# Kernel optimization log

Hardware: AMD Instinct MI355X
Metric: run time of the kernel (lower is better)

Reference implementation:

```python
import jax, jax.numpy as jnp
import numpy as np

N_NODES = 50000
N_EDGES = 1_600_000
FEAT, HIDDEN, NUM_CLASS = 128, 128, 64


def setup_inputs() -> dict:
    key = jax.random.key(0)
    k1, k2, k3, k4, k5 = jax.random.split(key, 5)
    h = jax.random.normal(k1, (N_NODES, FEAT), dtype=jnp.float32)
    edge_index = jax.random.randint(k2, (2, N_EDGES), 0, N_NODES, dtype=jnp.int32)
    # Glorot-ish init for the three GraphConv weights (bias=False)
    W1 = jax.random.normal(k3, (FEAT, HIDDEN), dtype=jnp.float32) * (1.0 / np.sqrt(FEAT))
    W2 = jax.random.normal(k4, (HIDDEN, HIDDEN), dtype=jnp.float32) * (1.0 / np.sqrt(HIDDEN))
    W3 = jax.random.normal(k5, (HIDDEN, NUM_CLASS), dtype=jnp.float32) * (1.0 / np.sqrt(HIDDEN))
    return {"h": h, "edge_index": edge_index, "W1": W1, "W2": W2, "W3": W3}


def _gcn_layer(h, W, src, dst, out_isqrt, in_isqrt, n_nodes):
    # DGL GraphConv, norm='both', bias=False: relu( D_in^{-1/2} A D_out^{-1/2} h W )
    h = h * out_isqrt[:, None]          # scale source features
    h = h @ W                            # dense projection (order-invariant)
    agg = jax.ops.segment_sum(h[src], dst, num_segments=n_nodes)  # SpMM aggregation
    agg = agg * in_isqrt[:, None]
    return jax.nn.relu(agg)


def reference(h, edge_index, W1, W2, W3):
    src, dst = edge_index[0], edge_index[1]
    ones = jnp.ones(src.shape[0], dtype=h.dtype)
    out_deg = jax.ops.segment_sum(ones, src, num_segments=N_NODES)
    in_deg = jax.ops.segment_sum(ones, dst, num_segments=N_NODES)
    out_isqrt = jnp.clip(out_deg, 1.0, None) ** -0.5
    in_isqrt = jnp.clip(in_deg, 1.0, None) ** -0.5
    h = _gcn_layer(h, W1, src, dst, out_isqrt, in_isqrt, N_NODES)
    h = _gcn_layer(h, W2, src, dst, out_isqrt, in_isqrt, N_NODES)
    h = _gcn_layer(h, W3, src, dst, out_isqrt, in_isqrt, N_NODES)
    return h
```

## Files before the change

kernel.cpp:

```cpp
#include <hip/hip_runtime.h>

#define N_NODES 50000
#define N_EDGES 1600000
#define FEAT 128
#define HIDDEN 128
#define NUM_CLASS 64

#define NBUCK 782
#define EPB 2048
#define NBLK 782
#define SCAP 2560
#define AGG_NBN 3125
#define GEMM_BLOCKS 782
#define NSHW 6256

typedef _Float16 h8 __attribute__((ext_vector_type(8)));
typedef _Float16 h4 __attribute__((ext_vector_type(4)));
typedef float f32x4 __attribute__((ext_vector_type(4)));

__global__ __launch_bounds__(256) void passA_kernel(const int* __restrict__ ei,
                                                    unsigned* __restrict__ priv,
                                                    int* __restrict__ localoff,
                                                    int* __restrict__ Cmat,
                                                    unsigned* __restrict__ nibshad) {
    __shared__ int cnt[1024];
    __shared__ int base[1024];
    __shared__ int cur[1024];
    __shared__ int tmp[256];
    __shared__ unsigned sorted[EPB];
    __shared__ unsigned nib[NSHW];
    const int t = threadIdx.x;
    const int blk = blockIdx.x;
    for (int i = t; i < 1024; i += 256) cnt[i] = 0;
    for (int i = t; i < NSHW; i += 256) nib[i] = 0;
    __syncthreads();

    const int ebase = blk * EPB;
    unsigned packed[8];
    int bk[8];
#pragma unroll
    for (int j = 0; j < 8; ++j) {
        const int e = ebase + t + j * 256;
        if (e < N_EDGES) {
            const unsigned s = (unsigned)ei[e];
            const unsigned d = (unsigned)ei[N_EDGES + e];
            bk[j] = (int)(d >> 6);
            packed[j] = s | ((d & 63u) << 16) | ((d >> 6) << 22);
            atomicAdd(&cnt[bk[j]], 1);
            atomicAdd(&nib[s >> 3], 1u << ((s & 7u) * 4u));
        } else bk[j] = -1;
    }
    __syncthreads();

    const int c0 = cnt[4*t], c1 = cnt[4*t+1], c2 = cnt[4*t+2], c3 = cnt[4*t+3];
    const int s = c0 + c1 + c2 + c3;
    tmp[t] = s;
    __syncthreads();
    for (int off = 1; off < 256; off <<= 1) {
        int v = (t >= off) ? tmp[t - off] : 0;
        __syncthreads();
        tmp[t] += v;
        __syncthreads();
    }
    const int excl = tmp[t] - s;
    base[4*t] = excl;            cur[4*t] = excl;
    base[4*t+1] = excl+c0;       cur[4*t+1] = excl+c0;
    base[4*t+2] = excl+c0+c1;    cur[4*t+2] = excl+c0+c1;
    base[4*t+3] = excl+c0+c1+c2; cur[4*t+3] = excl+c0+c1+c2;
    __syncthreads();

    for (int b = t; b < NBUCK; b += 256) {
        localoff[(size_t)blk * NBUCK + b] = base[b];
        Cmat[(size_t)blk * NBUCK + b] = cnt[b];
    }
#pragma unroll
    for (int j = 0; j < 8; ++j)
        if (bk[j] >= 0) {
            const int pos = atomicAdd(&cur[bk[j]], 1);
            sorted[pos] = packed[j];
        }
    __syncthreads();
    const int total = min(EPB, N_EDGES - ebase);
    for (int i = t; i < total; i += 256) priv[(size_t)blk * EPB + i] = sorted[i];
    unsigned* dst = nibshad + (size_t)blk * NSHW;
    for (int i = t; i < NSHW; i += 256) dst[i] = nib[i];
}

__global__ __launch_bounds__(256) void btotal_kernel(const int* __restrict__ Cmat,
                                                     int* __restrict__ total) {
    const int b0 = blockIdx.x * 4;
    const int t = threadIdx.x;
    const int c = t & 3, r = t >> 2;
    int s = 0;
    if (b0 + c < NBUCK)
        for (int i = r; i < NBLK; i += 64) s += Cmat[(size_t)i * NBUCK + b0 + c];
    __shared__ int red[256];
    red[t] = s;
    __syncthreads();
    for (int off = 128; off >= 4; off >>= 1) {
        if (t < off) red[t] += red[t + off];
        __syncthreads();
    }
    if (t < 4 && b0 + t < NBUCK) total[b0 + t] = red[t];
}

__global__ __launch_bounds__(256) void bscan2_kernel(const int* __restrict__ total,
                                                     int* __restrict__ csr_base,
                                                     int* __restrict__ row_off) {
    __shared__ int tt[1024];
    __shared__ int tmp[256];
    const int t = threadIdx.x;
    for (int i = t; i < 1024; i += 256) tt[i] = (i < NBUCK) ? total[i] : 0;
    __syncthreads();
    const int c0 = tt[4*t], c1 = tt[4*t+1], c2 = tt[4*t+2], c3 = tt[4*t+3];
    const int s = c0 + c1 + c2 + c3;
    tmp[t] = s;
    __syncthreads();
    for (int off = 1; off < 256; off <<= 1) {
        int v = (t >= off) ? tmp[t - off] : 0;
        __syncthreads();
        tmp[t] += v;
        __syncthreads();
    }
    const int excl = tmp[t] - s;
    if (4*t < NBUCK)   csr_base[4*t]   = excl;
    if (4*t+1 < NBUCK) csr_base[4*t+1] = excl + c0;
    if (4*t+2 < NBUCK) csr_base[4*t+2] = excl + c0 + c1;
    if (4*t+3 < NBUCK) csr_base[4*t+3] = excl + c0 + c1 + c2;
    if (t == 0) { csr_base[NBUCK] = N_EDGES; row_off[N_NODES] = N_EDGES; }
}

__global__ __launch_bounds__(256) void setup_kernel(const float* __restrict__ W1,
                                                    const float* __restrict__ W2,
                                                    const float* __restrict__ W3,
                                                    _Float16* __restrict__ WhT,
                                                    const unsigned* __restrict__ nibshad,
                                                    float* __restrict__ out_isqrt) {
    const int bid = blockIdx.x;
    const int t = threadIdx.x;
    if (bid < 160) {
        const int id = bid * 256 + t;
        if (id < 16384) {
            const int n = id >> 7, k = id & 127;
            WhT[id] = (_Float16)W1[k * 128 + n];
        } else if (id < 32768) {
            const int i = id - 16384, n = i >> 7, k = i & 127;
            WhT[id] = (_Float16)W2[k * 128 + n];
        } else if (id < 40960) {
            const int i = id - 32768, n = i >> 7, k = i & 127;
            WhT[id] = (_Float16)W3[k * 64 + n];
        }
        return;
    }
    const int blk = bid - 160;
    const int w0 = blk * 8;
    const int wl = t & 7, c = t >> 3;
    int acc[8] = {0, 0, 0, 0, 0, 0, 0, 0};
    for (int sh = c; sh < NBLK; sh += 32) {
        const unsigned u = nibshad[(size_t)sh * NSHW + w0 + wl];
        acc[0] += u & 15u;         acc[1] += (u >> 4) & 15u;
        acc[2] += (u >> 8) & 15u;  acc[3] += (u >> 12) & 15u;
        acc[4] += (u >> 16) & 15u; acc[5] += (u >> 20) & 15u;
        acc[6] += (u >> 24) & 15u; acc[7] += (u >> 28);
    }
    __shared__ int red[32][8][8];
#pragma unroll
    for (int nb = 0; nb < 8; ++nb) red[c][wl][nb] = acc[nb];
    __syncthreads();
    for (int off = 16; off > 0; off >>= 1) {
        if (c < off) {
#pragma unroll
            for (int nb = 0; nb < 8; ++nb) red[c][wl][nb] += red[c + off][wl][nb];
        }
        __syncthreads();
    }
    if (t < 64) {
        const int wl2 = t >> 3, nb = t & 7;
        const int node = (w0 + wl2) * 8 + nb;
        if (node < N_NODES) {
            const int d = red[0][wl2][nb];
            out_isqrt[node] = rsqrtf((float)(d < 1 ? 1 : d));
        }
    }
}

__global__ __launch_bounds__(256) void csr2_kernel(const int* __restrict__ localoff,
                                                   const unsigned* __restrict__ priv,
                                                   const int* __restrict__ csr_base,
                                                   unsigned short* __restrict__ csr,
                                                   int* __restrict__ row_off,
                                                   float* __restrict__ in_isqrt) {
    __shared__ unsigned gath[SCAP];
    __shared__ int tmp[256];
    __shared__ int cnt64[64];
    __shared__ int cur64[64];
    const int b = blockIdx.x;
    const int t = threadIdx.x;

    int off_[4], len_[4];
#pragma unroll
    for (int u = 0; u < 4; ++u) {
        const int blk = 4*t + u;
        if (blk < NBLK) {
            const int o = localoff[(size_t)blk * NBUCK + b];
            const int nxt = (b == NBUCK - 1) ? min(EPB, N_EDGES - blk * EPB)
                                             : localoff[(size_t)blk * NBUCK + b + 1];
            off_[u] = o; len_[u] = nxt - o;
        } else { off_[u] = 0; len_[u] = 0; }
    }
    const int s = len_[0] + len_[1] + len_[2] + len_[3];
    tmp[t] = s;
    __syncthreads();
    for (int off = 1; off < 256; off <<= 1) {
        int v = (t >= off) ? tmp[t - off] : 0;
        __syncthreads();
        tmp[t] += v;
        __syncthreads();
    }
    int run = tmp[t] - s;
    const int total = tmp[255];
#pragma unroll
    for (int u = 0; u < 4; ++u) {
        const int blk = 4*t + u;
        const unsigned* srcp = priv + (size_t)blk * EPB + off_[u];
        for (int j = 0; j < len_[u]; ++j)
            if (run + j < SCAP) gath[run + j] = srcp[j];
        run += len_[u];
    }
    if (t < 64) cnt64[t] = 0;
    __syncthreads();

    const int gtot = min(total, SCAP);
    for (int i = t; i < gtot; i += 256) atomicAdd(&cnt64[(gath[i] >> 16) & 63u], 1);
    __syncthreads();

    const int v64 = (t < 64) ? cnt64[t] : 0;
    tmp[t] = v64;
    __syncthreads();
    for (int off = 1; off < 64; off <<= 1) {
        int v = (t >= off) ? tmp[t - off] : 0;
        __syncthreads();
        tmp[t] += v;
        __syncthreads();
    }
    if (t < 64) {
        const int myoff = csr_base[b] + tmp[t] - v64;
        cur64[t] = myoff;
        const int node = b * 64 + t;
        if (node < N_NODES) {
            row_off[node] = myoff;
            in_isqrt[node] = rsqrtf((float)(v64 > 0 ? v64 : 1));
        }
    }
    __syncthreads();

    for (int i = t; i < gtot; i += 256) {
        const unsigned w = gath[i];
        const int pos = atomicAdd(&cur64[(w >> 16) & 63u], 1);
        csr[pos] = (unsigned short)(w & 0xFFFFu);
    }
}

template <int OUT, typename InT>
__global__ __launch_bounds__(256) void gemm_kernel(const InT* __restrict__ H,
                                                   const _Float16* __restrict__ WhT,
                                                   const float* __restrict__ out_isqrt,
                                                   _Float16* __restrict__ Ys) {
    constexpr int NT = OUT / 16;
    __shared__ _Float16 Hs[64 * 128];
    char* hb = (char*)Hs;
    const int tid = threadIdx.x;
    const int bn = blockIdx.x * 64;

    {
        const int n = tid & 63, kg = tid >> 6;
        const int gn = bn + n;
        const int swz = (n & 7) << 4;
        if (gn < N_NODES) {
            if constexpr (sizeof(InT) == 4) {
                const float4* hrow = (const float4*)(H + (size_t)gn * FEAT) + kg * 8;
#pragma unroll
                for (int jj = 0; jj < 4; ++jj) {
                    const float4 u = hrow[jj * 2];
                    const float4 v = hrow[jj * 2 + 1];
                    h8 r;
                    r[0] = (_Float16)u.x; r[1] = (_Float16)u.y; r[2] = (_Float16)u.z; r[3] = (_Float16)u.w;
                    r[4] = (_Float16)v.x; r[5] = (_Float16)v.y; r[6] = (_Float16)v.z; r[7] = (_Float16)v.w;
                    *(h8*)(hb + ((n * 256 + kg * 64 + jj * 16) ^ swz)) = r;
                }
            } else {
                const h8* hrow = (const h8*)(H + (size_t)gn * FEAT) + kg * 4;
#pragma unroll
                for (int jj = 0; jj < 4; ++jj)
                    *(h8*)(hb + ((n * 256 + kg * 64 + jj * 16) ^ swz)) = hrow[jj];
            }
        } else {
            h8 z;
#pragma unroll
            for (int i = 0; i < 8; ++i) z[i] = (_Float16)0.f;
#pragma unroll
            for (int jj = 0; jj < 4; ++jj)
                *(h8*)(hb + ((n * 256 + kg * 64 + jj * 16) ^ swz)) = z;
        }
    }
    __syncthreads();

    const int l = tid & 63, w = tid >> 6;
    const int lm = l & 15, lk = l >> 4;
    const int nloc = w * 16 + lm;
    const int swzr = (nloc & 7) << 4;

    h8 bfrag[4];
#pragma unroll
    for (int kt = 0; kt < 4; ++kt)
        bfrag[kt] = *(const h8*)(hb + ((nloc * 256 + (lk * 8 + kt * 32) * 2) ^ swzr));

    f32x4 acc[NT];
#pragma unroll
    for (int nt = 0; nt < NT; ++nt) acc[nt] = (f32x4){0.f, 0.f, 0.f, 0.f};

#pragma unroll
    for (int nt = 0; nt < NT; ++nt) {
        const _Float16* wp = WhT + (size_t)(nt * 16 + lm) * 128 + lk * 8;
#pragma unroll
        for (int kt = 0; kt < 4; ++kt) {
            const h8 afrag = *(const h8*)(wp + kt * 32);
            acc[nt] = __builtin_amdgcn_mfma_f32_16x16x32_f16(afrag, bfrag[kt], acc[nt], 0, 0, 0);
        }
    }

    const int node = bn + w * 16 + lm;
    if (node < N_NODES) {
        const float sc = out_isqrt[node];
#pragma unroll
        for (int nt = 0; nt < NT; ++nt) {
            const int f0 = nt * 16 + lk * 4;
            h4 r;
            r[0] = (_Float16)(acc[nt][0] * sc);
            r[1] = (_Float16)(acc[nt][1] * sc);
            r[2] = (_Float16)(acc[nt][2] * sc);
            r[3] = (_Float16)(acc[nt][3] * sc);
            *(h4*)(Ys + ((size_t)(f0 >> 5) * N_NODES + node) * 32 + (f0 & 31)) = r;
        }
    }
}

template <int F, typename OT>
__global__ __launch_bounds__(256) void agg_kernel(const int* __restrict__ row_off,
                                                  const unsigned short* __restrict__ csr,
                                                  const _Float16* __restrict__ Ys,
                                                  const float* __restrict__ in_isqrt,
                                                  OT* __restrict__ out) {
    constexpr int NS = F / 32;
    const int s  = blockIdx.x & (NS - 1);
    const int nb = blockIdx.x / NS;
    const int tid = threadIdx.x;
    const int lane = tid & 63;
    const int j = lane >> 4;
    const int esub = (lane >> 2) & 3;
    const int q = lane & 3;

    const int d = nb * 16 + (tid >> 6) * 4 + j;
    const _Float16* Yp = Ys + (size_t)s * (N_NODES * 32) + q * 8;

    const int end = row_off[d + 1];
    float a0 = 0.f, a1 = 0.f, a2 = 0.f, a3 = 0.f, a4 = 0.f, a5 = 0.f, a6 = 0.f, a7 = 0.f;

    int e = row_off[d] + esub;
    for (; e + 12 < end; e += 16) {
        const int i0 = csr[e];
        const int i1 = csr[e + 4];
        const int i2 = csr[e + 8];
        const int i3 = csr[e + 12];
        const h8 v0 = *(const h8*)(Yp + (size_t)i0 * 32);
        const h8 v1 = *(const h8*)(Yp + (size_t)i1 * 32);
        const h8 v2 = *(const h8*)(Yp + (size_t)i2 * 32);
        const h8 v3 = *(const h8*)(Yp + (size_t)i3 * 32);
        a0 += (float)v0[0] + (float)v1[0] + (float)v2[0] + (float)v3[0];
        a1 += (float)v0[1] + (float)v1[1] + (float)v2[1] + (float)v3[1];
        a2 += (float)v0[2] + (float)v1[2] + (float)v2[2] + (float)v3[2];
        a3 += (float)v0[3] + (float)v1[3] + (float)v2[3] + (float)v3[3];
        a4 += (float)v0[4] + (float)v1[4] + (float)v2[4] + (float)v3[4];
        a5 += (float)v0[5] + (float)v1[5] + (float)v2[5] + (float)v3[5];
        a6 += (float)v0[6] + (float)v1[6] + (float)v2[6] + (float)v3[6];
        a7 += (float)v0[7] + (float)v1[7] + (float)v2[7] + (float)v3[7];
    }
    for (; e + 4 < end; e += 8) {
        const int i0 = csr[e];
        const int i1 = csr[e + 4];
        const h8 v0 = *(const h8*)(Yp + (size_t)i0 * 32);
        const h8 v1 = *(const h8*)(Yp + (size_t)i1 * 32);
        a0 += (float)v0[0] + (float)v1[0];
        a1 += (float)v0[1] + (float)v1[1];
        a2 += (float)v0[2] + (float)v1[2];
        a3 += (float)v0[3] + (float)v1[3];
        a4 += (float)v0[4] + (float)v1[4];
        a5 += (float)v0[5] + (float)v1[5];
        a6 += (float)v0[6] + (float)v1[6];
        a7 += (float)v0[7] + (float)v1[7];
    }
    if (e < end) {
        const int i0 = csr[e];
        const h8 v0 = *(const h8*)(Yp + (size_t)i0 * 32);
        a0 += (float)v0[0]; a1 += (float)v0[1]; a2 += (float)v0[2]; a3 += (float)v0[3];
        a4 += (float)v0[4]; a5 += (float)v0[5]; a6 += (float)v0[6]; a7 += (float)v0[7];
    }

    a0 += __shfl_xor(a0, 4, 64); a0 += __shfl_xor(a0, 8, 64);
    a1 += __shfl_xor(a1, 4, 64); a1 += __shfl_xor(a1, 8, 64);
    a2 += __shfl_xor(a2, 4, 64); a2 += __shfl_xor(a2, 8, 64);
    a3 += __shfl_xor(a3, 4, 64); a3 += __shfl_xor(a3, 8, 64);
    a4 += __shfl_xor(a4, 4, 64); a4 += __shfl_xor(a4, 8, 64);
    a5 += __shfl_xor(a5, 4, 64); a5 += __shfl_xor(a5, 8, 64);
    a6 += __shfl_xor(a6, 4, 64); a6 += __shfl_xor(a6, 8, 64);
    a7 += __shfl_xor(a7, 4, 64); a7 += __shfl_xor(a7, 8, 64);

    if (esub == 0) {
        const float isq = in_isqrt[d];
        const float r0 = fmaxf(a0 * isq, 0.f), r1 = fmaxf(a1 * isq, 0.f);
        const float r2 = fmaxf(a2 * isq, 0.f), r3 = fmaxf(a3 * isq, 0.f);
        const float r4 = fmaxf(a4 * isq, 0.f), r5 = fmaxf(a5 * isq, 0.f);
        const float r6 = fmaxf(a6 * isq, 0.f), r7 = fmaxf(a7 * isq, 0.f);
        if constexpr (sizeof(OT) == 2) {
            h8 o;
            o[0] = (_Float16)r0; o[1] = (_Float16)r1; o[2] = (_Float16)r2; o[3] = (_Float16)r3;
            o[4] = (_Float16)r4; o[5] = (_Float16)r5; o[6] = (_Float16)r6; o[7] = (_Float16)r7;
            *(h8*)((_Float16*)out + (size_t)d * F + s * 32 + q * 8) = o;
        } else {
            float* op = (float*)out + (size_t)d * F + s * 32 + q * 8;
            float4 w0 = {r0, r1, r2, r3}, w1 = {r4, r5, r6, r7};
            *(float4*)op = w0;
            *(float4*)(op + 4) = w1;
        }
    }
}

extern "C" void kernel_launch(void* const* d_in, const int* in_sizes, int n_in,
                              void* d_out, int out_size, void* d_ws, size_t ws_size,
                              hipStream_t stream) {
    const float* h  = (const float*)d_in[0];
    const int*   ei = (const int*)d_in[1];
    const float* W1 = (const float*)d_in[2];
    const float* W2 = (const float*)d_in[3];
    const float* W3 = (const float*)d_in[4];
    float* out = (float*)d_out;

    char* p = (char*)d_ws;
    auto alloc = [&p](size_t bytes) {
        void* r = (void*)p;
        p += (bytes + 255) & ~(size_t)255;
        return r;
    };
    int*   row_off  = (int*)alloc((N_NODES + 1) * sizeof(int));
    int*   csr_base = (int*)alloc((NBUCK + 1) * sizeof(int));
    int*   total    = (int*)alloc(NBUCK * sizeof(int));
    unsigned short* csr = (unsigned short*)alloc((size_t)N_EDGES * sizeof(unsigned short));
    float* in_isqrt  = (float*)alloc(N_NODES * sizeof(float));
    float* out_isqrt = (float*)alloc(N_NODES * sizeof(float));
    _Float16* WhT   = (_Float16*)alloc(40960 * sizeof(_Float16));
    _Float16* Ys    = (_Float16*)alloc((size_t)N_NODES * HIDDEN * sizeof(_Float16));
    _Float16* bufA  = (_Float16*)alloc((size_t)N_NODES * HIDDEN * sizeof(_Float16));
    _Float16* bufB  = (_Float16*)alloc((size_t)N_NODES * HIDDEN * sizeof(_Float16));
    unsigned* nibshad = (unsigned*)alloc((size_t)NBLK * NSHW * sizeof(unsigned));
    unsigned* priv   = (unsigned*)bufA;
    int* localoff    = (int*)bufB;
    int* Cmat        = localoff + (size_t)NBLK * NBUCK;

    passA_kernel<<<NBLK, 256, 0, stream>>>(ei, priv, localoff, Cmat, nibshad);
    btotal_kernel<<<(NBUCK + 3) / 4, 256, 0, stream>>>(Cmat, total);
    bscan2_kernel<<<1, 256, 0, stream>>>(total, csr_base, row_off);
    setup_kernel<<<160 + NBLK, 256, 0, stream>>>(W1, W2, W3, WhT, nibshad, out_isqrt);
    csr2_kernel<<<NBUCK, 256, 0, stream>>>(localoff, priv, csr_base, csr, row_off, in_isqrt);

    gemm_kernel<HIDDEN, float><<<GEMM_BLOCKS, 256, 0, stream>>>(h, WhT, out_isqrt, Ys);
    agg_kernel<HIDDEN, _Float16><<<4 * AGG_NBN, 256, 0, stream>>>(row_off, csr, Ys, in_isqrt, bufA);

    gemm_kernel<HIDDEN, _Float16><<<GEMM_BLOCKS, 256, 0, stream>>>(bufA, WhT + 16384, out_isqrt, Ys);
    agg_kernel<HIDDEN, _Float16><<<4 * AGG_NBN, 256, 0, stream>>>(row_off, csr, Ys, in_isqrt, bufB);

    gemm_kernel<NUM_CLASS, _Float16><<<GEMM_BLOCKS, 256, 0, stream>>>(bufB, WhT + 32768, out_isqrt, Ys);
    agg_kernel<NUM_CLASS, float><<<2 * AGG_NBN, 256, 0, stream>>>(row_off, csr, Ys, in_isqrt, out);
}
```

Baseline: 235.2 us.

## Widen feature slabs to 64 halfs and fold bucket totals into setup kernel

The intermediate Ys layout changes from 32-wide to 64-wide feature slabs. Each aggregation gather now reads a 128-byte contiguous row segment, and each dst node is handled by 32 lanes (8 feature quads × 4 edge subsets) instead of 16. The 16-edge unrolled loop is dropped, and the grid shrinks to match. Separately, the btotal kernel is merged into setup_kernel as extra blocks so there is one fewer launch, with bscan2 run after it. The aims are better gather coalescing and less launch overhead, at the cost of less memory-level parallelism per thread.

Result: slower. 241.6 us (+2.8%).

```diff
diff --git a/kernel.cpp b/kernel.cpp
--- a/kernel.cpp
+++ b/kernel.cpp
@@ -10,7 +10,7 @@
 #define EPB 2048
 #define NBLK 782
 #define SCAP 2560
-#define AGG_NBN 3125
+#define AGG_NBN 6250
 #define GEMM_BLOCKS 782
 #define NSHW 6256
 
@@ -86,51 +86,9 @@
     for (int i = t; i < NSHW; i += 256) dst[i] = nib[i];
 }
 
-__global__ __launch_bounds__(256) void btotal_kernel(const int* __restrict__ Cmat,
-                                                     int* __restrict__ total) {
-    const int b0 = blockIdx.x * 4;
-    const int t = threadIdx.x;
-    const int c = t & 3, r = t >> 2;
-    int s = 0;
-    if (b0 + c < NBUCK)
-        for (int i = r; i < NBLK; i += 64) s += Cmat[(size_t)i * NBUCK + b0 + c];
-    __shared__ int red[256];
-    red[t] = s;
-    __syncthreads();
-    for (int off = 128; off >= 4; off >>= 1) {
-        if (t < off) red[t] += red[t + off];
-        __syncthreads();
-    }
-    if (t < 4 && b0 + t < NBUCK) total[b0 + t] = red[t];
-}
-
-__global__ __launch_bounds__(256) void bscan2_kernel(const int* __restrict__ total,
-                                                     int* __restrict__ csr_base,
-                                                     int* __restrict__ row_off) {
-    __shared__ int tt[1024];
-    __shared__ int tmp[256];
-    const int t = threadIdx.x;
-    for (int i = t; i < 1024; i += 256) tt[i] = (i < NBUCK) ? total[i] : 0;
-    __syncthreads();
-    const int c0 = tt[4*t], c1 = tt[4*t+1], c2 = tt[4*t+2], c3 = tt[4*t+3];
-    const int s = c0 + c1 + c2 + c3;
-    tmp[t] = s;
-    __syncthreads();
-    for (int off = 1; off < 256; off <<= 1) {
-        int v = (t >= off) ? tmp[t - off] : 0;
-        __syncthreads();
-        tmp[t] += v;
-        __syncthreads();
-    }
-    const int excl = tmp[t] - s;
-    if (4*t < NBUCK)   csr_base[4*t]   = excl;
-    if (4*t+1 < NBUCK) csr_base[4*t+1] = excl + c0;
-    if (4*t+2 < NBUCK) csr_base[4*t+2] = excl + c0 + c1;
-    if (4*t+3 < NBUCK) csr_base[4*t+3] = excl + c0 + c1 + c2;
-    if (t == 0) { csr_base[NBUCK] = N_EDGES; row_off[N_NODES] = N_EDGES; }
-}
-
-__global__ __launch_bounds__(256) void setup_kernel(const float* __restrict__ W1,
+__global__ __launch_bounds__(256) void setup_kernel(const int* __restrict__ Cmat,
+                                                    int* __restrict__ total,
+                                                    const float* __restrict__ W1,
                                                     const float* __restrict__ W2,
                                                     const float* __restrict__ W3,
                                                     _Float16* __restrict__ WhT,
@@ -138,8 +96,24 @@
                                                     float* __restrict__ out_isqrt) {
     const int bid = blockIdx.x;
     const int t = threadIdx.x;
-    if (bid < 160) {
-        const int id = bid * 256 + t;
+    if (bid < 196) {
+        const int b0 = bid * 4;
+        const int c = t & 3, r = t >> 2;
+        int s = 0;
+        if (b0 + c < NBUCK)
+            for (int i = r; i < NBLK; i += 64) s += Cmat[(size_t)i * NBUCK + b0 + c];
+        __shared__ int red[256];
+        red[t] = s;
+        __syncthreads();
+        for (int off = 128; off >= 4; off >>= 1) {
+            if (t < off) red[t] += red[t + off];
+            __syncthreads();
+        }
+        if (t < 4 && b0 + t < NBUCK) total[b0 + t] = red[t];
+        return;
+    }
+    if (bid < 356) {
+        const int id = (bid - 196) * 256 + t;
         if (id < 16384) {
             const int n = id >> 7, k = id & 127;
             WhT[id] = (_Float16)W1[k * 128 + n];
@@ -152,7 +126,7 @@
         }
         return;
     }
-    const int blk = bid - 160;
+    const int blk = bid - 356;
     const int w0 = blk * 8;
     const int wl = t & 7, c = t >> 3;
     int acc[8] = {0, 0, 0, 0, 0, 0, 0, 0};
@@ -163,14 +137,14 @@
         acc[4] += (u >> 16) & 15u; acc[5] += (u >> 20) & 15u;
         acc[6] += (u >> 24) & 15u; acc[7] += (u >> 28);
     }
-    __shared__ int red[32][8][8];
-#pragma unroll
-    for (int nb = 0; nb < 8; ++nb) red[c][wl][nb] = acc[nb];
+    __shared__ int red2[32][8][8];
+#pragma unroll
+    for (int nb = 0; nb < 8; ++nb) red2[c][wl][nb] = acc[nb];
     __syncthreads();
     for (int off = 16; off > 0; off >>= 1) {
         if (c < off) {
 #pragma unroll
-            for (int nb = 0; nb < 8; ++nb) red[c][wl][nb] += red[c + off][wl][nb];
+            for (int nb = 0; nb < 8; ++nb) red2[c][wl][nb] += red2[c + off][wl][nb];
         }
         __syncthreads();
     }
@@ -178,10 +152,36 @@
         const int wl2 = t >> 3, nb = t & 7;
         const int node = (w0 + wl2) * 8 + nb;
         if (node < N_NODES) {
-            const int d = red[0][wl2][nb];
+            const int d = red2[0][wl2][nb];
             out_isqrt[node] = rsqrtf((float)(d < 1 ? 1 : d));
         }
     }
+}
+
+__global__ __launch_bounds__(256) void bscan2_kernel(const int* __restrict__ total,
+                                                     int* __restrict__ csr_base,
+                                                     int* __restrict__ row_off) {
+    __shared__ int tt[1024];
+    __shared__ int tmp[256];
+    const int t = threadIdx.x;
+    for (int i = t; i < 1024; i += 256) tt[i] = (i < NBUCK) ? total[i] : 0;
+    __syncthreads();
+    const int c0 = tt[4*t], c1 = tt[4*t+1], c2 = tt[4*t+2], c3 = tt[4*t+3];
+    const int s = c0 + c1 + c2 + c3;
+    tmp[t] = s;
+    __syncthreads();
+    for (int off = 1; off < 256; off <<= 1) {
+        int v = (t >= off) ? tmp[t - off] : 0;
+        __syncthreads();
+        tmp[t] += v;
+        __syncthreads();
+    }
+    const int excl = tmp[t] - s;
+    if (4*t < NBUCK)   csr_base[4*t]   = excl;
+    if (4*t+1 < NBUCK) csr_base[4*t+1] = excl + c0;
+    if (4*t+2 < NBUCK) csr_base[4*t+2] = excl + c0 + c1;
+    if (4*t+3 < NBUCK) csr_base[4*t+3] = excl + c0 + c1 + c2;
+    if (t == 0) { csr_base[NBUCK] = N_EDGES; row_off[N_NODES] = N_EDGES; }
 }
 
 __global__ __launch_bounds__(256) void csr2_kernel(const int* __restrict__ localoff,
@@ -340,7 +340,7 @@
             r[1] = (_Float16)(acc[nt][1] * sc);
             r[2] = (_Float16)(acc[nt][2] * sc);
             r[3] = (_Float16)(acc[nt][3] * sc);
-            *(h4*)(Ys + ((size_t)(f0 >> 5) * N_NODES + node) * 32 + (f0 & 31)) = r;
+            *(h4*)(Ys + ((size_t)(f0 >> 6) * N_NODES + node) * 64 + (f0 & 63)) = r;
         }
     }
 }
@@ -351,45 +351,27 @@
                                                   const _Float16* __restrict__ Ys,
                                                   const float* __restrict__ in_isqrt,
                                                   OT* __restrict__ out) {
-    constexpr int NS = F / 32;
+    constexpr int NS = F / 64;
     const int s  = blockIdx.x & (NS - 1);
     const int nb = blockIdx.x / NS;
     const int tid = threadIdx.x;
     const int lane = tid & 63;
-    const int j = lane >> 4;
-    const int esub = (lane >> 2) & 3;
-    const int q = lane & 3;
-
-    const int d = nb * 16 + (tid >> 6) * 4 + j;
-    const _Float16* Yp = Ys + (size_t)s * (N_NODES * 32) + q * 8;
+    const int q = lane & 7;
+    const int esub = (lane >> 3) & 3;
+    const int j = lane >> 5;
+
+    const int d = nb * 8 + (tid >> 6) * 2 + j;
+    const _Float16* Yp = Ys + (size_t)s * (N_NODES * 64) + q * 8;
 
     const int end = row_off[d + 1];
     float a0 = 0.f, a1 = 0.f, a2 = 0.f, a3 = 0.f, a4 = 0.f, a5 = 0.f, a6 = 0.f, a7 = 0.f;
 
     int e = row_off[d] + esub;
-    for (; e + 12 < end; e += 16) {
-        const int i0 = csr[e];
-        const int i1 = csr[e + 4];
-        const int i2 = csr[e + 8];
-        const int i3 = csr[e + 12];
-        const h8 v0 = *(const h8*)(Yp + (size_t)i0 * 32);
-        const h8 v1 = *(const h8*)(Yp + (size_t)i1 * 32);
-        const h8 v2 = *(const h8*)(Yp + (size_t)i2 * 32);
-        const h8 v3 = *(const h8*)(Yp + (size_t)i3 * 32);
-        a0 += (float)v0[0] + (float)v1[0] + (float)v2[0] + (float)v3[0];
-        a1 += (float)v0[1] + (float)v1[1] + (float)v2[1] + (float)v3[1];
-        a2 += (float)v0[2] + (float)v1[2] + (float)v2[2] + (float)v3[2];
-        a3 += (float)v0[3] + (float)v1[3] + (float)v2[3] + (float)v3[3];
-        a4 += (float)v0[4] + (float)v1[4] + (float)v2[4] + (float)v3[4];
-        a5 += (float)v0[5] + (float)v1[5] + (float)v2[5] + (float)v3[5];
-        a6 += (float)v0[6] + (float)v1[6] + (float)v2[6] + (float)v3[6];
-        a7 += (float)v0[7] + (float)v1[7] + (float)v2[7] + (float)v3[7];
-    }
     for (; e + 4 < end; e += 8) {
         const int i0 = csr[e];
         const int i1 = csr[e + 4];
-        const h8 v0 = *(const h8*)(Yp + (size_t)i0 * 32);
-        const h8 v1 = *(const h8*)(Yp + (size_t)i1 * 32);
+        const h8 v0 = *(const h8*)(Yp + (size_t)i0 * 64);
+        const h8 v1 = *(const h8*)(Yp + (size_t)i1 * 64);
         a0 += (float)v0[0] + (float)v1[0];
         a1 += (float)v0[1] + (float)v1[1];
         a2 += (float)v0[2] + (float)v1[2];
@@ -401,19 +383,19 @@
     }
     if (e < end) {
         const int i0 = csr[e];
-        const h8 v0 = *(const h8*)(Yp + (size_t)i0 * 32);
+        const h8 v0 = *(const h8*)(Yp + (size_t)i0 * 64);
         a0 += (float)v0[0]; a1 += (float)v0[1]; a2 += (float)v0[2]; a3 += (float)v0[3];
         a4 += (float)v0[4]; a5 += (float)v0[5]; a6 += (float)v0[6]; a7 += (float)v0[7];
     }
 
-    a0 += __shfl_xor(a0, 4, 64); a0 += __shfl_xor(a0, 8, 64);
-    a1 += __shfl_xor(a1, 4, 64); a1 += __shfl_xor(a1, 8, 64);
-    a2 += __shfl_xor(a2, 4, 64); a2 += __shfl_xor(a2, 8, 64);
-    a3 += __shfl_xor(a3, 4, 64); a3 += __shfl_xor(a3, 8, 64);
-    a4 += __shfl_xor(a4, 4, 64); a4 += __shfl_xor(a4, 8, 64);
-    a5 += __shfl_xor(a5, 4, 64); a5 += __shfl_xor(a5, 8, 64);
-    a6 += __shfl_xor(a6, 4, 64); a6 += __shfl_xor(a6, 8, 64);
-    a7 += __shfl_xor(a7, 4, 64); a7 += __shfl_xor(a7, 8, 64);
+    a0 += __shfl_xor(a0, 8, 64); a0 += __shfl_xor(a0, 16, 64);
+    a1 += __shfl_xor(a1, 8, 64); a1 += __shfl_xor(a1, 16, 64);
+    a2 += __shfl_xor(a2, 8, 64); a2 += __shfl_xor(a2, 16, 64);
+    a3 += __shfl_xor(a3, 8, 64); a3 += __shfl_xor(a3, 16, 64);
+    a4 += __shfl_xor(a4, 8, 64); a4 += __shfl_xor(a4, 16, 64);
+    a5 += __shfl_xor(a5, 8, 64); a5 += __shfl_xor(a5, 16, 64);
+    a6 += __shfl_xor(a6, 8, 64); a6 += __shfl_xor(a6, 16, 64);
+    a7 += __shfl_xor(a7, 8, 64); a7 += __shfl_xor(a7, 16, 64);
 
     if (esub == 0) {
         const float isq = in_isqrt[d];
@@ -425,9 +407,9 @@
             h8 o;
             o[0] = (_Float16)r0; o[1] = (_Float16)r1; o[2] = (_Float16)r2; o[3] = (_Float16)r3;
             o[4] = (_Float16)r4; o[5] = (_Float16)r5; o[6] = (_Float16)r6; o[7] = (_Float16)r7;
-            *(h8*)((_Float16*)out + (size_t)d * F + s * 32 + q * 8) = o;
+            *(h8*)((_Float16*)out + (size_t)d * F + s * 64 + q * 8) = o;
         } else {
-            float* op = (float*)out + (size_t)d * F + s * 32 + q * 8;
+            float* op = (float*)out + (size_t)d * F + s * 64 + q * 8;
             float4 w0 = {r0, r1, r2, r3}, w1 = {r4, r5, r6, r7};
             *(float4*)op = w0;
             *(float4*)(op + 4) = w1;
@@ -467,17 +449,16 @@
     int* Cmat        = localoff + (size_t)NBLK * NBUCK;
 
     passA_kernel<<<NBLK, 256, 0, stream>>>(ei, priv, localoff, Cmat, nibshad);
-    btotal_kernel<<<(NBUCK + 3) / 4, 256, 0, stream>>>(Cmat, total);
+    setup_kernel<<<1138, 256, 0, stream>>>(Cmat, total, W1, W2, W3, WhT, nibshad, out_isqrt);
     bscan2_kernel<<<1, 256, 0, stream>>>(total, csr_base, row_off);
-    setup_kernel<<<160 + NBLK, 256, 0, stream>>>(W1, W2, W3, WhT, nibshad, out_isqrt);
     csr2_kernel<<<NBUCK, 256, 0, stream>>>(localoff, priv, csr_base, csr, row_off, in_isqrt);
 
     gemm_kernel<HIDDEN, float><<<GEMM_BLOCKS, 256, 0, stream>>>(h, WhT, out_isqrt, Ys);
-    agg_kernel<HIDDEN, _Float16><<<4 * AGG_NBN, 256, 0, stream>>>(row_off, csr, Ys, in_isqrt, bufA);
+    agg_kernel<HIDDEN, _Float16><<<2 * AGG_NBN, 256, 0, stream>>>(row_off, csr, Ys, in_isqrt, bufA);
 
     gemm_kernel<HIDDEN, _Float16><<<GEMM_BLOCKS, 256, 0, stream>>>(bufA, WhT + 16384, out_isqrt, Ys);
-    agg_kernel<HIDDEN, _Float16><<<4 * AGG_NBN, 256, 0, stream>>>(row_off, csr, Ys, in_isqrt, bufB);
+    agg_kernel<HIDDEN, _Float16><<<2 * AGG_NBN, 256, 0, stream>>>(row_off, csr, Ys, in_isqrt, bufB);
 
     gemm_kernel<NUM_CLASS, _Float16><<<GEMM_BLOCKS, 256, 0, stream>>>(bufB, WhT + 32768, out_isqrt, Ys);
-    agg_kernel<NUM_CLASS, float><<<2 * AGG_NBN, 256, 0, stream>>>(row_off, csr, Ys, in_isqrt, out);
-}
+    agg_kernel<NUM_CLASS, float><<<AGG_NBN, 256, 0, stream>>>(row_off, csr, Ys, in_isqrt, out);
+}
```

## Merge preprocessing kernels and co-schedule CSR build with first GEMM

Applied to the files above, without the earlier changes.

Reduces the preprocessing pipeline from six launches to three. Weight conversion moves into extra blocks of passA, the bucket-total reduction moves into setup_kernel, and the single-block bucket scan becomes a per-block redundant scan inside a combined CSR-build plus first-layer GEMM kernel. The aim is to remove launch gaps and serial tiny kernels, and to overlap the CSR scatter with the first projection. The cost is that every CSR block redoes the 782-entry scan, and the shared-memory sizing is now common to both roles.

New measurement: 216.2 us. -8.1%, faster.

```diff
diff --git a/kernel.cpp b/kernel.cpp
--- a/kernel.cpp
+++ b/kernel.cpp
@@ -22,15 +22,33 @@
                                                     unsigned* __restrict__ priv,
                                                     int* __restrict__ localoff,
                                                     int* __restrict__ Cmat,
-                                                    unsigned* __restrict__ nibshad) {
+                                                    unsigned* __restrict__ nibshad,
+                                                    const float* __restrict__ W1,
+                                                    const float* __restrict__ W2,
+                                                    const float* __restrict__ W3,
+                                                    _Float16* __restrict__ WhT) {
+    const int t = threadIdx.x;
+    const int blk = blockIdx.x;
+    if (blk >= NBLK) {
+        const int id = (blk - NBLK) * 256 + t;
+        if (id < 16384) {
+            const int n = id >> 7, k = id & 127;
+            WhT[id] = (_Float16)W1[k * 128 + n];
+        } else if (id < 32768) {
+            const int i = id - 16384, n = i >> 7, k = i & 127;
+            WhT[id] = (_Float16)W2[k * 128 + n];
+        } else if (id < 40960) {
+            const int i = id - 32768, n = i >> 7, k = i & 127;
+            WhT[id] = (_Float16)W3[k * 64 + n];
+        }
+        return;
+    }
     __shared__ int cnt[1024];
     __shared__ int base[1024];
     __shared__ int cur[1024];
     __shared__ int tmp[256];
     __shared__ unsigned sorted[EPB];
     __shared__ unsigned nib[NSHW];
-    const int t = threadIdx.x;
-    const int blk = blockIdx.x;
     for (int i = t; i < 1024; i += 256) cnt[i] = 0;
     for (int i = t; i < NSHW; i += 256) nib[i] = 0;
     __syncthreads();
@@ -86,73 +104,29 @@
     for (int i = t; i < NSHW; i += 256) dst[i] = nib[i];
 }
 
-__global__ __launch_bounds__(256) void btotal_kernel(const int* __restrict__ Cmat,
-                                                     int* __restrict__ total) {
-    const int b0 = blockIdx.x * 4;
-    const int t = threadIdx.x;
-    const int c = t & 3, r = t >> 2;
-    int s = 0;
-    if (b0 + c < NBUCK)
-        for (int i = r; i < NBLK; i += 64) s += Cmat[(size_t)i * NBUCK + b0 + c];
-    __shared__ int red[256];
-    red[t] = s;
-    __syncthreads();
-    for (int off = 128; off >= 4; off >>= 1) {
-        if (t < off) red[t] += red[t + off];
-        __syncthreads();
-    }
-    if (t < 4 && b0 + t < NBUCK) total[b0 + t] = red[t];
-}
-
-__global__ __launch_bounds__(256) void bscan2_kernel(const int* __restrict__ total,
-                                                     int* __restrict__ csr_base,
-                                                     int* __restrict__ row_off) {
-    __shared__ int tt[1024];
-    __shared__ int tmp[256];
-    const int t = threadIdx.x;
-    for (int i = t; i < 1024; i += 256) tt[i] = (i < NBUCK) ? total[i] : 0;
-    __syncthreads();
-    const int c0 = tt[4*t], c1 = tt[4*t+1], c2 = tt[4*t+2], c3 = tt[4*t+3];
-    const int s = c0 + c1 + c2 + c3;
-    tmp[t] = s;
-    __syncthreads();
-    for (int off = 1; off < 256; off <<= 1) {
-        int v = (t >= off) ? tmp[t - off] : 0;
-        __syncthreads();
-        tmp[t] += v;
-        __syncthreads();
-    }
-    const int excl = tmp[t] - s;
-    if (4*t < NBUCK)   csr_base[4*t]   = excl;
-    if (4*t+1 < NBUCK) csr_base[4*t+1] = excl + c0;
-    if (4*t+2 < NBUCK) csr_base[4*t+2] = excl + c0 + c1;
-    if (4*t+3 < NBUCK) csr_base[4*t+3] = excl + c0 + c1 + c2;
-    if (t == 0) { csr_base[NBUCK] = N_EDGES; row_off[N_NODES] = N_EDGES; }
-}
-
-__global__ __launch_bounds__(256) void setup_kernel(const float* __restrict__ W1,
-                                                    const float* __restrict__ W2,
-                                                    const float* __restrict__ W3,
-                                                    _Float16* __restrict__ WhT,
+__global__ __launch_bounds__(256) void setup_kernel(const int* __restrict__ Cmat,
+                                                    int* __restrict__ total,
                                                     const unsigned* __restrict__ nibshad,
                                                     float* __restrict__ out_isqrt) {
     const int bid = blockIdx.x;
     const int t = threadIdx.x;
-    if (bid < 160) {
-        const int id = bid * 256 + t;
-        if (id < 16384) {
-            const int n = id >> 7, k = id & 127;
-            WhT[id] = (_Float16)W1[k * 128 + n];
-        } else if (id < 32768) {
-            const int i = id - 16384, n = i >> 7, k = i & 127;
-            WhT[id] = (_Float16)W2[k * 128 + n];
-        } else if (id < 40960) {
-            const int i = id - 32768, n = i >> 7, k = i & 127;
-            WhT[id] = (_Float16)W3[k * 64 + n];
-        }
+    if (bid < 196) {
+        const int b0 = bid * 4;
+        const int c = t & 3, r = t >> 2;
+        int s = 0;
+        if (b0 + c < NBUCK)
+            for (int i = r; i < NBLK; i += 64) s += Cmat[(size_t)i * NBUCK + b0 + c];
+        __shared__ int red[256];
+        red[t] = s;
+        __syncthreads();
+        for (int off = 128; off >= 4; off >>= 1) {
+            if (t < off) red[t] += red[t + off];
+            __syncthreads();
+        }
+        if (t < 4 && b0 + t < NBUCK) total[b0 + t] = red[t];
         return;
     }
-    const int blk = bid - 160;
+    const int blk = bid - 196;
     const int w0 = blk * 8;
     const int wl = t & 7, c = t >> 3;
     int acc[8] = {0, 0, 0, 0, 0, 0, 0, 0};
@@ -163,14 +137,14 @@
         acc[4] += (u >> 16) & 15u; acc[5] += (u >> 20) & 15u;
         acc[6] += (u >> 24) & 15u; acc[7] += (u >> 28);
     }
-    __shared__ int red[32][8][8];
-#pragma unroll
-    for (int nb = 0; nb < 8; ++nb) red[c][wl][nb] = acc[nb];
+    __shared__ int red2[32][8][8];
+#pragma unroll
+    for (int nb = 0; nb < 8; ++nb) red2[c][wl][nb] = acc[nb];
     __syncthreads();
     for (int off = 16; off > 0; off >>= 1) {
         if (c < off) {
 #pragma unroll
-            for (int nb = 0; nb < 8; ++nb) red[c][wl][nb] += red[c + off][wl][nb];
+            for (int nb = 0; nb < 8; ++nb) red2[c][wl][nb] += red2[c + off][wl][nb];
         }
         __syncthreads();
     }
@@ -178,99 +152,22 @@
         const int wl2 = t >> 3, nb = t & 7;
         const int node = (w0 + wl2) * 8 + nb;
         if (node < N_NODES) {
-            const int d = red[0][wl2][nb];
+            const int d = red2[0][wl2][nb];
             out_isqrt[node] = rsqrtf((float)(d < 1 ? 1 : d));
         }
     }
 }
 
-__global__ __launch_bounds__(256) void csr2_kernel(const int* __restrict__ localoff,
-                                                   const unsigned* __restrict__ priv,
-                                                   const int* __restrict__ csr_base,
-                                                   unsigned short* __restrict__ csr,
-                                                   int* __restrict__ row_off,
-                                                   float* __restrict__ in_isqrt) {
-    __shared__ unsigned gath[SCAP];
-    __shared__ int tmp[256];
-    __shared__ int cnt64[64];
-    __shared__ int cur64[64];
-    const int b = blockIdx.x;
-    const int t = threadIdx.x;
-
-    int off_[4], len_[4];
-#pragma unroll
-    for (int u = 0; u < 4; ++u) {
-        const int blk = 4*t + u;
-        if (blk < NBLK) {
-            const int o = localoff[(size_t)blk * NBUCK + b];
-            const int nxt = (b == NBUCK - 1) ? min(EPB, N_EDGES - blk * EPB)
-                                             : localoff[(size_t)blk * NBUCK + b + 1];
-            off_[u] = o; len_[u] = nxt - o;
-        } else { off_[u] = 0; len_[u] = 0; }
-    }
-    const int s = len_[0] + len_[1] + len_[2] + len_[3];
-    tmp[t] = s;
-    __syncthreads();
-    for (int off = 1; off < 256; off <<= 1) {
-        int v = (t >= off) ? tmp[t - off] : 0;
-        __syncthreads();
-        tmp[t] += v;
-        __syncthreads();
-    }
-    int run = tmp[t] - s;
-    const int total = tmp[255];
-#pragma unroll
-    for (int u = 0; u < 4; ++u) {
-        const int blk = 4*t + u;
-        const unsigned* srcp = priv + (size_t)blk * EPB + off_[u];
-        for (int j = 0; j < len_[u]; ++j)
-            if (run + j < SCAP) gath[run + j] = srcp[j];
-        run += len_[u];
-    }
-    if (t < 64) cnt64[t] = 0;
-    __syncthreads();
-
-    const int gtot = min(total, SCAP);
-    for (int i = t; i < gtot; i += 256) atomicAdd(&cnt64[(gath[i] >> 16) & 63u], 1);
-    __syncthreads();
-
-    const int v64 = (t < 64) ? cnt64[t] : 0;
-    tmp[t] = v64;
-    __syncthreads();
-    for (int off = 1; off < 64; off <<= 1) {
-        int v = (t >= off) ? tmp[t - off] : 0;
-        __syncthreads();
-        tmp[t] += v;
-        __syncthreads();
-    }
-    if (t < 64) {
-        const int myoff = csr_base[b] + tmp[t] - v64;
-        cur64[t] = myoff;
-        const int node = b * 64 + t;
-        if (node < N_NODES) {
-            row_off[node] = myoff;
-            in_isqrt[node] = rsqrtf((float)(v64 > 0 ? v64 : 1));
-        }
-    }
-    __syncthreads();
-
-    for (int i = t; i < gtot; i += 256) {
-        const unsigned w = gath[i];
-        const int pos = atomicAdd(&cur64[(w >> 16) & 63u], 1);
-        csr[pos] = (unsigned short)(w & 0xFFFFu);
-    }
-}
-
 template <int OUT, typename InT>
-__global__ __launch_bounds__(256) void gemm_kernel(const InT* __restrict__ H,
-                                                   const _Float16* __restrict__ WhT,
-                                                   const float* __restrict__ out_isqrt,
-                                                   _Float16* __restrict__ Ys) {
+__device__ __forceinline__ void gemm_body(const InT* __restrict__ H,
+                                          const _Float16* __restrict__ WhT,
+                                          const float* __restrict__ out_isqrt,
+                                          _Float16* __restrict__ Ys,
+                                          const int bidx, const int tid,
+                                          _Float16* Hs) {
     constexpr int NT = OUT / 16;
-    __shared__ _Float16 Hs[64 * 128];
     char* hb = (char*)Hs;
-    const int tid = threadIdx.x;
-    const int bn = blockIdx.x * 64;
+    const int bn = bidx * 64;
 
     {
         const int n = tid & 63, kg = tid >> 6;
@@ -342,6 +239,127 @@
             r[3] = (_Float16)(acc[nt][3] * sc);
             *(h4*)(Ys + ((size_t)(f0 >> 5) * N_NODES + node) * 32 + (f0 & 31)) = r;
         }
+    }
+}
+
+template <int OUT, typename InT>
+__global__ __launch_bounds__(256) void gemm_kernel(const InT* __restrict__ H,
+                                                   const _Float16* __restrict__ WhT,
+                                                   const float* __restrict__ out_isqrt,
+                                                   _Float16* __restrict__ Ys) {
+    __shared__ _Float16 Hs[64 * 128];
+    gemm_body<OUT, InT>(H, WhT, out_isqrt, Ys, blockIdx.x, threadIdx.x, Hs);
+}
+
+__global__ __launch_bounds__(256) void csr2gemm_kernel(const int* __restrict__ localoff,
+                                                       const unsigned* __restrict__ priv,
+                                                       const int* __restrict__ total,
+                                                       unsigned short* __restrict__ csr,
+                                                       int* __restrict__ row_off,
+                                                       float* __restrict__ in_isqrt,
+                                                       const float* __restrict__ H,
+                                                       const _Float16* __restrict__ WhT,
+                                                       const float* __restrict__ out_isqrt,
+                                                       _Float16* __restrict__ Ys) {
+    __shared__ char smem[16384];
+    const int bid = blockIdx.x;
+    const int t = threadIdx.x;
+    if (bid >= NBUCK) {
+        gemm_body<HIDDEN, float>(H, WhT, out_isqrt, Ys, bid - NBUCK, t, (_Float16*)smem);
+        return;
+    }
+    int* tmp = (int*)smem;
+    unsigned* gath = (unsigned*)(smem + 1024);
+    int* cnt64 = (int*)(smem + 1024 + SCAP * 4);
+    int* cur64 = cnt64 + 64;
+    const int b = bid;
+
+    {
+        const int g = 4 * t;
+        const int s0 = (g < NBUCK) ? total[g] : 0;
+        const int s1 = (g + 1 < NBUCK) ? total[g + 1] : 0;
+        const int s2 = (g + 2 < NBUCK) ? total[g + 2] : 0;
+        const int s3 = (g + 3 < NBUCK) ? total[g + 3] : 0;
+        const int s = s0 + s1 + s2 + s3;
+        tmp[t] = s;
+        __syncthreads();
+        for (int off = 1; off < 256; off <<= 1) {
+            int v = (t >= off) ? tmp[t - off] : 0;
+            __syncthreads();
+            tmp[t] += v;
+            __syncthreads();
+        }
+        const int excl = tmp[t] - s;
+        __syncthreads();
+        tmp[t] = excl;
+        __syncthreads();
+    }
+    int cb = tmp[b >> 2];
+    for (int u = (b & ~3); u < b; ++u) cb += total[u];
+    __syncthreads();
+
+    int off_[4], len_[4];
+#pragma unroll
+    for (int u = 0; u < 4; ++u) {
+        const int blk = 4 * t + u;
+        if (blk < NBLK) {
+            const int o = localoff[(size_t)blk * NBUCK + b];
+            const int nxt = (b == NBUCK - 1) ? min(EPB, N_EDGES - blk * EPB)
+                                             : localoff[(size_t)blk * NBUCK + b + 1];
+            off_[u] = o; len_[u] = nxt - o;
+        } else { off_[u] = 0; len_[u] = 0; }
+    }
+    const int s = len_[0] + len_[1] + len_[2] + len_[3];
+    tmp[t] = s;
+    __syncthreads();
+    for (int off = 1; off < 256; off <<= 1) {
+        int v = (t >= off) ? tmp[t - off] : 0;
+        __syncthreads();
+        tmp[t] += v;
+        __syncthreads();
+    }
+    int run = tmp[t] - s;
+    const int totalE = tmp[255];
+#pragma unroll
+    for (int u = 0; u < 4; ++u) {
+        const int blk = 4 * t + u;
+        const unsigned* srcp = priv + (size_t)blk * EPB + off_[u];
+        for (int j = 0; j < len_[u]; ++j)
+            if (run + j < SCAP) gath[run + j] = srcp[j];
+        run += len_[u];
+    }
+    if (t < 64) cnt64[t] = 0;
+    __syncthreads();
+
+    const int gtot = min(totalE, SCAP);
+    for (int i = t; i < gtot; i += 256) atomicAdd(&cnt64[(gath[i] >> 16) & 63u], 1);
+    __syncthreads();
+
+    const int v64 = (t < 64) ? cnt64[t] : 0;
+    tmp[t] = v64;
+    __syncthreads();
+    for (int off = 1; off < 64; off <<= 1) {
+        int v = (t >= off) ? tmp[t - off] : 0;
+        __syncthreads();
+        tmp[t] += v;
+        __syncthreads();
+    }
+    if (t < 64) {
+        const int myoff = cb + tmp[t] - v64;
+        cur64[t] = myoff;
+        const int node = b * 64 + t;
+        if (node < N_NODES) {
+            row_off[node] = myoff;
+            in_isqrt[node] = rsqrtf((float)(v64 > 0 ? v64 : 1));
+        }
+    }
+    if (bid == 0 && t == 0) row_off[N_NODES] = N_EDGES;
+    __syncthreads();
+
+    for (int i = t; i < gtot; i += 256) {
+        const unsigned w = gath[i];
+        const int pos = atomicAdd(&cur64[(w >> 16) & 63u], 1);
+        csr[pos] = (unsigned short)(w & 0xFFFFu);
     }
 }
 
@@ -452,7 +470,6 @@
         return r;
     };
     int*   row_off  = (int*)alloc((N_NODES + 1) * sizeof(int));
-    int*   csr_base = (int*)alloc((NBUCK + 1) * sizeof(int));
     int*   total    = (int*)alloc(NBUCK * sizeof(int));
     unsigned short* csr = (unsigned short*)alloc((size_t)N_EDGES * sizeof(unsigned short));
     float* in_isqrt  = (float*)alloc(N_NODES * sizeof(float));
@@ -466,13 +483,13 @@
     int* localoff    = (int*)bufB;
     int* Cmat        = localoff + (size_t)NBLK * NBUCK;
 
-    passA_kernel<<<NBLK, 256, 0, stream>>>(ei, priv, localoff, Cmat, nibshad);
-    btotal_kernel<<<(NBUCK + 3) / 4, 256, 0, stream>>>(Cmat, total);
-    bscan2_kernel<<<1, 256, 0, stream>>>(total, csr_base, row_off);
-    setup_kernel<<<160 + NBLK, 256, 0, stream>>>(W1, W2, W3, WhT, nibshad, out_isqrt);
-    csr2_kernel<<<NBUCK, 256, 0, stream>>>(localoff, priv, csr_base, csr, row_off, in_isqrt);
-
-    gemm_kernel<HIDDEN, float><<<GEMM_BLOCKS, 256, 0, stream>>>(h, WhT, out_isqrt, Ys);
+    passA_kernel<<<NBLK + 160, 256, 0, stream>>>(ei, priv, localoff, Cmat, nibshad,
+                                                 W1, W2, W3, WhT);
+    setup_kernel<<<978, 256, 0, stream>>>(Cmat, total, nibshad, out_isqrt);
+    csr2gemm_kernel<<<NBUCK + GEMM_BLOCKS, 256, 0, stream>>>(localoff, priv, total,
+                                                             csr, row_off, in_isqrt,
+                                                             h, WhT, out_isqrt, Ys);
+
     agg_kernel<HIDDEN, _Float16><<<4 * AGG_NBN, 256, 0, stream>>>(row_off, csr, Ys, in_isqrt, bufA);
 
     gemm_kernel<HIDDEN, _Float16><<<GEMM_BLOCKS, 256, 0, stream>>>(bufA, WhT + 16384, out_isqrt, Ys);
```
